# Optimization experiments

Measured on AMD Instinct MI355X. Metric: run time of the kernel, lower is better.

The kernel has to match this reference:

```python
import jax, jax.numpy as jnp
import numpy as np

WINDOW = 16  # hardcoded in module __init__

B, S, E, H = 2, 2048, 1024, 16
HD = E // H


def setup_inputs() -> dict:
    key = jax.random.key(0)
    k1, k2, k3, k4, k5, k6 = jax.random.split(key, 6)
    input_embeddings = jax.random.normal(k1, (B, S, E), dtype=jnp.float32)
    token_ids = jax.random.randint(k2, (B, S), 0, 32000, dtype=jnp.int64)
    # nn.MultiheadAttention parameters: packed in_proj (3E, E) + bias, out_proj (E, E) + bias
    in_proj_weight = jax.random.normal(k3, (3 * E, E), dtype=jnp.float32) * 0.02
    in_proj_bias = jax.random.normal(k4, (3 * E,), dtype=jnp.float32) * 0.02
    out_proj_weight = jax.random.normal(k5, (E, E), dtype=jnp.float32) * 0.02
    out_proj_bias = jax.random.normal(k6, (E,), dtype=jnp.float32) * 0.02
    return {
        "input_embeddings": input_embeddings,
        "token_ids": token_ids,
        "in_proj_weight": in_proj_weight,
        "in_proj_bias": in_proj_bias,
        "out_proj_weight": out_proj_weight,
        "out_proj_bias": out_proj_bias,
    }


def _blocked_mask(seq_len: int) -> jnp.ndarray:
    # Module sets mask[i, j] = True for j in [i - WINDOW, i] (17 positions).
    # PyTorch bool attn_mask: True = NOT allowed to attend.
    i = jnp.arange(seq_len)[:, None]
    j = jnp.arange(seq_len)[None, :]
    return (j <= i) & (j >= i - WINDOW)  # [S, S] bool, True = masked out


def reference(input_embeddings, token_ids, in_proj_weight, in_proj_bias,
              out_proj_weight, out_proj_bias):
    x = input_embeddings  # [B, S, E]
    b, s, e = x.shape
    # Packed QKV projection (torch Linear: y = x W^T + b)
    qkv = jnp.einsum('bse,fe->bsf', x, in_proj_weight) + in_proj_bias  # [B, S, 3E]
    q, k, v = jnp.split(qkv, 3, axis=-1)
    # Split heads: [B, H, S, HD]
    q = q.reshape(b, s, H, HD).transpose(0, 2, 1, 3)
    k = k.reshape(b, s, H, HD).transpose(0, 2, 1, 3)
    v = v.reshape(b, s, H, HD).transpose(0, 2, 1, 3)
    scale = 1.0 / jnp.sqrt(jnp.asarray(HD, dtype=x.dtype))
    scores = jnp.einsum('bhqd,bhkd->bhqk', q * scale, k)  # [B, H, S, S]
    blocked = _blocked_mask(s)  # True = masked
    scores = jnp.where(blocked[None, None, :, :], -jnp.inf, scores)
    attn = jax.nn.softmax(scores, axis=-1)
    ctx = jnp.einsum('bhqk,bhkd->bhqd', attn, v)  # [B, H, S, HD]
    ctx = ctx.transpose(0, 2, 1, 3).reshape(b, s, e)
    out = jnp.einsum('bse,fe->bsf', ctx, out_proj_weight) + out_proj_bias
    return out
```

## Files before the change

### kernel.cpp

```cpp
#include <hip/hip_runtime.h>

typedef __attribute__((ext_vector_type(8))) __bf16 bf16x8;
typedef __attribute__((ext_vector_type(4))) float f32x4;
typedef unsigned short u16;
typedef unsigned int u32;

#define MFMA16(a, b, c) __builtin_amdgcn_mfma_f32_16x16x32_bf16((a), (b), (c), 0, 0, 0)

__device__ __forceinline__ u16 f2bf(float f) {
  return (u16)((__float_as_uint(f) + 0x8000u) >> 16);
}

#define BDIM 2
#define SDIM 2048
#define EDIM 1024
#define HDIM 16
#define HD 64
#define MDIM (BDIM * SDIM)

#define SC_C1 0.1803368801111355f

typedef __attribute__((address_space(3))) void lds_void;
typedef __attribute__((address_space(1))) void g_void;

__device__ __forceinline__ void async_lds16(const void* g, void* lds_byte) {
  __builtin_amdgcn_global_load_lds((const g_void*)g, (lds_void*)lds_byte, 16, 0, 0);
}

__global__ __launch_bounds__(256) void cvt3_kernel(
    const float* __restrict__ s0, u16* __restrict__ d0, int n0,
    const float* __restrict__ s1, u16* __restrict__ d1, int n1,
    const float* __restrict__ s2, u16* __restrict__ d2, int n2) {
  int i = (blockIdx.x * 256 + threadIdx.x) * 8;
  const float* s;
  u16* d;
  if (i < n0) {
    s = s0 + i; d = d0 + i;
  } else if (i < n0 + n1) {
    s = s1 + (i - n0); d = d1 + (i - n0);
  } else if (i < n0 + n1 + n2) {
    s = s2 + (i - n0 - n1); d = d2 + (i - n0 - n1);
  } else {
    return;
  }
  float4 f0 = *(const float4*)(s);
  float4 f1 = *(const float4*)(s + 4);
  union { uint4 u; u16 h[8]; } o;
  o.h[0] = f2bf(f0.x); o.h[1] = f2bf(f0.y); o.h[2] = f2bf(f0.z); o.h[3] = f2bf(f0.w);
  o.h[4] = f2bf(f1.x); o.h[5] = f2bf(f1.y); o.h[6] = f2bf(f1.z); o.h[7] = f2bf(f1.w);
  *(uint4*)(d) = o.u;
}

__global__ __launch_bounds__(256) void gemm_qkv_kernel(
    const u16* __restrict__ X, const u16* __restrict__ W,
    const float* __restrict__ bias, u16* __restrict__ qb,
    u16* __restrict__ kb, u16* __restrict__ vtb) {
  __shared__ __align__(16) u16 As[128 * 64];
  __shared__ __align__(16) u16 Bs[128 * 64];
  const int m0 = blockIdx.x * 128, n0 = blockIdx.y * 128;
  const bool isV = (n0 >= 2 * EDIM);
  const int t = threadIdx.x;
  const int l = t & 63;
  const int quad = l >> 4, col = l & 15;
  const int wid = t >> 6;
  const int mh = wid & 1, nh = wid >> 1;
  const int wofs = (t & 192) << 4;
  f32x4 acc[4][4] = {};
  const u16* Ab = X + (size_t)m0 * EDIM;
  const u16* Bb = W + (size_t)n0 * EDIM;
  char* AsB = (char*)As;
  char* BsB = (char*)Bs;

  for (int k0 = 0; k0 < EDIM; k0 += 64) {
    __syncthreads();
#pragma unroll
    for (int p = 0; p < 4; p++) {
      int idx = p * 256 + t;
      int row = idx >> 3;
      int gch = (idx & 7) ^ (row & 7);
      async_lds16(Ab + (size_t)row * EDIM + k0 + gch * 8, AsB + p * 4096 + wofs);
      async_lds16(Bb + (size_t)row * EDIM + k0 + gch * 8, BsB + p * 4096 + wofs);
    }
    __syncthreads();
#pragma unroll
    for (int kk = 0; kk < 2; kk++) {
      bf16x8 af[4], bfr[4];
#pragma unroll
      for (int i = 0; i < 4; i++) {
        int ra = 64 * mh + 16 * i + col;
        af[i] = *(const bf16x8*)&As[ra * 64 + (((kk * 4 + quad) ^ (ra & 7)) * 8)];
        int rb = 64 * nh + 16 * i + col;
        bfr[i] = *(const bf16x8*)&Bs[rb * 64 + (((kk * 4 + quad) ^ (rb & 7)) * 8)];
      }
      if (isV) {
#pragma unroll
        for (int i = 0; i < 4; i++)
#pragma unroll
          for (int j = 0; j < 4; j++)
            acc[i][j] = MFMA16(bfr[i], af[j], acc[i][j]);
      } else {
#pragma unroll
        for (int i = 0; i < 4; i++)
#pragma unroll
          for (int j = 0; j < 4; j++)
            acc[i][j] = MFMA16(af[i], bfr[j], acc[i][j]);
      }
    }
  }

  if (isV) {
#pragma unroll
    for (int i = 0; i < 4; i++)
#pragma unroll
      for (int j = 0; j < 4; j++)
#pragma unroll
        for (int r = 0; r < 4; r++) {
          int n = n0 + 64 * nh + 16 * i + quad * 4 + r;
          int m = m0 + 64 * mh + 16 * j + col;
          float val = acc[i][j][r] + bias[n];
          int e = n & 1023;
          int hh = e >> 6, d = e & 63;
          int bb = m >> 11, s = m & 2047;
          vtb[(((size_t)(bb * HDIM + hh)) * HD + d) * SDIM + s] = f2bf(val);
        }
  } else {
    const float qscale = (n0 < EDIM) ? SC_C1 : 1.0f;
#pragma unroll
    for (int i = 0; i < 4; i++)
#pragma unroll
      for (int j = 0; j < 4; j++)
#pragma unroll
        for (int r = 0; r < 4; r++) {
          int m = m0 + 64 * mh + 16 * i + quad * 4 + r;
          int n = n0 + 64 * nh + 16 * j + col;
          float val = (acc[i][j][r] + bias[n]) * qscale;
          int which = n >> 10, e = n & 1023;
          int hh = e >> 6, d = e & 63;
          int bb = m >> 11, s = m & 2047;
          u16* dst = (which == 0) ? qb : kb;
          dst[(((size_t)(bb * HDIM + hh)) * SDIM + s) * HD + d] = f2bf(val);
        }
  }
}

__global__ __launch_bounds__(256) void attn_kernel(
    const u16* __restrict__ qg, const u16* __restrict__ kg,
    const u16* __restrict__ vtg, u16* __restrict__ ctx) {
  __shared__ __align__(16) u16 KB[2][64 * 64];
  __shared__ __align__(16) u16 VB[3][64 * 64];
  __shared__ __align__(16) u16 Ps[64 * 68];

  const int bh = blockIdx.x;
  const int q0 = blockIdx.y * 64;
  const int t = threadIdx.x;
  const int wid = t >> 6, l = t & 63;
  const int quad = l >> 4, col = l & 15;
  const size_t base = (size_t)bh * SDIM * HD;

  bf16x8 aq[2];
  {
    const u16* qp = qg + base + (size_t)(q0 + 16 * wid + col) * HD + quad * 8;
    aq[0] = *(const bf16x8*)(qp);
    aq[1] = *(const bf16x8*)(qp + 32);
  }
  const int qrow = q0 + 16 * wid + quad * 4;

  const int srow = t >> 3;
  const int g = (t & 7) ^ (srow & 7);
  const u16* kptr = kg + base + (size_t)srow * HD + g * 8;
  const u16* vptr = vtg + base + (size_t)srow * SDIM + g * 8;
  const int wofs = (t & 192) << 4;

  auto stageK = [&](int kt, int buf) {
    char* d = (char*)KB[buf] + wofs;
    async_lds16(kptr + (size_t)(kt * 64) * HD, d);
    async_lds16(kptr + (size_t)(kt * 64 + 32) * HD, d + 4096);
  };
  auto stageV = [&](int kt, int buf) {
    char* d = (char*)VB[buf] + wofs;
    async_lds16(vptr + kt * 64, d);
    async_lds16(vptr + (size_t)32 * SDIM + kt * 64, d + 4096);
  };
  auto qkt = [&](const u16* Kt, f32x4* sco) {
#pragma unroll
    for (int half = 0; half < 2; half++)
#pragma unroll
      for (int ct = 0; ct < 4; ct++) {
        int r = 16 * ct + col;
        int phys = (4 * half + quad) ^ (r & 7);
        bf16x8 bfrag = *(const bf16x8*)&Kt[r * 64 + phys * 8];
        sco[ct] = MFMA16(aq[half], bfrag, sco[ct]);
      }
  };

  float psum[4] = {};
  f32x4 oacc[4] = {};
  f32x4 sc[4] = {}, scn[4];

  const int NT = SDIM / 64;
  stageK(0, 0);
  stageV(0, 0);
  __syncthreads();
  qkt(KB[0], sc);
  stageK(1, 1);
  stageV(1, 1);

  int vb_n = 2;
  for (int kt = 0; kt < NT; kt++) {
    __syncthreads();
    if (kt + 1 < NT) {
#pragma unroll
      for (int ct = 0; ct < 4; ct++) scn[ct] = f32x4{0.f, 0.f, 0.f, 0.f};
      qkt(KB[(kt + 1) & 1], scn);
    }
    if (kt + 2 < NT) {
      stageK(kt + 2, kt & 1);
      stageV(kt + 2, vb_n);
    }
    vb_n = (vb_n == 2) ? 0 : vb_n + 1;

    const int k0 = kt * 64;
    const int pbase = (16 * wid + quad * 4) * 68 + col;
    if (k0 <= q0 + 63 && k0 + 63 >= q0 - 16) {
#pragma unroll
      for (int ct = 0; ct < 4; ct++)
#pragma unroll
        for (int r = 0; r < 4; r++) {
          int i = qrow + r, j = k0 + 16 * ct + col;
          float arg = (j <= i && j + 16 >= i) ? -1.0e30f : sc[ct][r];
          float p = __builtin_exp2f(arg);
          psum[r] += p;
          Ps[pbase + r * 68 + 16 * ct] = f2bf(p);
        }
    } else {
#pragma unroll
      for (int ct = 0; ct < 4; ct++)
#pragma unroll
        for (int r = 0; r < 4; r++) {
          float p = __builtin_exp2f(sc[ct][r]);
          psum[r] += p;
          Ps[pbase + r * 68 + 16 * ct] = f2bf(p);
        }
    }

    const u16* Vt = VB[kt % 3];
#pragma unroll
    for (int half = 0; half < 2; half++) {
      bf16x8 pa =
          *(const bf16x8*)&Ps[(16 * wid + col) * 68 + half * 32 + quad * 8];
#pragma unroll
      for (int dt = 0; dt < 4; dt++) {
        int vr = 16 * dt + col;
        int phys = (4 * half + quad) ^ (vr & 7);
        bf16x8 vbf = *(const bf16x8*)&Vt[vr * 64 + phys * 8];
        oacc[dt] = MFMA16(pa, vbf, oacc[dt]);
      }
    }
#pragma unroll
    for (int ct = 0; ct < 4; ct++) sc[ct] = scn[ct];
  }

#pragma unroll
  for (int off = 1; off < 16; off <<= 1)
#pragma unroll
    for (int r = 0; r < 4; r++) psum[r] += __shfl_xor(psum[r], off, 64);

  const int b = bh >> 4, h = bh & 15;
  float linv[4];
#pragma unroll
  for (int r = 0; r < 4; r++) linv[r] = 1.0f / psum[r];
#pragma unroll
  for (int dt = 0; dt < 4; dt++)
#pragma unroll
    for (int r = 0; r < 4; r++) {
      int qgl = qrow + r;
      int d = 16 * dt + col;
      ctx[((size_t)(b * SDIM + qgl)) * EDIM + h * HD + d] =
          f2bf(oacc[dt][r] * linv[r]);
    }
}

__global__ __launch_bounds__(256) void gemm_out_kernel(
    const u16* __restrict__ A, const u16* __restrict__ W,
    const float* __restrict__ bias, float* __restrict__ out) {
  __shared__ __align__(16) u16 As[128 * 64];
  __shared__ __align__(16) u16 Bs[128 * 64];
  const int m0 = blockIdx.x * 128, n0 = blockIdx.y * 128;
  const int t = threadIdx.x;
  const int l = t & 63;
  const int quad = l >> 4, col = l & 15;
  const int wid = t >> 6;
  const int mh = wid & 1, nh = wid >> 1;
  const int wofs = (t & 192) << 4;
  f32x4 acc[4][4] = {};
  const u16* Ab = A + (size_t)m0 * EDIM;
  const u16* Bb = W + (size_t)n0 * EDIM;
  char* AsB = (char*)As;
  char* BsB = (char*)Bs;

  for (int k0 = 0; k0 < EDIM; k0 += 64) {
    __syncthreads();
#pragma unroll
    for (int p = 0; p < 4; p++) {
      int idx = p * 256 + t;
      int row = idx >> 3;
      int gch = (idx & 7) ^ (row & 7);
      async_lds16(Ab + (size_t)row * EDIM + k0 + gch * 8, AsB + p * 4096 + wofs);
      async_lds16(Bb + (size_t)row * EDIM + k0 + gch * 8, BsB + p * 4096 + wofs);
    }
    __syncthreads();
#pragma unroll
    for (int kk = 0; kk < 2; kk++) {
      bf16x8 af[4], bfr[4];
#pragma unroll
      for (int i = 0; i < 4; i++) {
        int ra = 64 * mh + 16 * i + col;
        af[i] = *(const bf16x8*)&As[ra * 64 + (((kk * 4 + quad) ^ (ra & 7)) * 8)];
        int rb = 64 * nh + 16 * i + col;
        bfr[i] = *(const bf16x8*)&Bs[rb * 64 + (((kk * 4 + quad) ^ (rb & 7)) * 8)];
      }
#pragma unroll
      for (int i = 0; i < 4; i++)
#pragma unroll
        for (int j = 0; j < 4; j++)
          acc[i][j] = MFMA16(af[i], bfr[j], acc[i][j]);
    }
  }

#pragma unroll
  for (int i = 0; i < 4; i++)
#pragma unroll
    for (int j = 0; j < 4; j++)
#pragma unroll
      for (int r = 0; r < 4; r++) {
        int m = m0 + 64 * mh + 16 * i + quad * 4 + r;
        int n = n0 + 64 * nh + 16 * j + col;
        out[(size_t)m * EDIM + n] = acc[i][j][r] + bias[n];
      }
}

extern "C" void kernel_launch(void* const* d_in, const int* in_sizes, int n_in,
                              void* d_out, int out_size, void* d_ws,
                              size_t ws_size, hipStream_t stream) {
  const float* x = (const float*)d_in[0];
  const float* in_w = (const float*)d_in[2];
  const float* in_b = (const float*)d_in[3];
  const float* out_w = (const float*)d_in[4];
  const float* out_b = (const float*)d_in[5];
  float* out = (float*)d_out;

  char* ws = (char*)d_ws;
  u16* Xb  = (u16*)ws;
  u16* ctx = (u16*)ws;
  u16* qb  = (u16*)(ws + (size_t)( 8 << 20));
  u16* kb  = (u16*)(ws + (size_t)(16 << 20));
  u16* vtb = (u16*)(ws + (size_t)(24 << 20));
  u16* Wib = (u16*)(ws + (size_t)(32 << 20));
  u16* Wob = (u16*)(ws + (size_t)(38 << 20));

  const int nX = MDIM * EDIM;
  const int nWi = 3 * EDIM * EDIM;
  const int nWo = EDIM * EDIM;
  cvt3_kernel<<<(nX + nWi + nWo) / 8 / 256, 256, 0, stream>>>(
      x, Xb, nX, in_w, Wib, nWi, out_w, Wob, nWo);

  gemm_qkv_kernel<<<dim3(MDIM / 128, 3 * EDIM / 128), 256, 0, stream>>>(
      Xb, Wib, in_b, qb, kb, vtb);
  attn_kernel<<<dim3(BDIM * HDIM, SDIM / 64), 256, 0, stream>>>(qb, kb, vtb, ctx);
  gemm_out_kernel<<<dim3(MDIM / 128, EDIM / 128), 256, 0, stream>>>(
      ctx, Wob, out_b, out);
}
```

Measured before the change: 215.1 us.

## Transpose QK^T MFMA, swizzle P tile, double-buffer V, ping-pong score registers

The QK^T MFMA operands are swapped, so each lane holds scores for a single query row. The softmax row sum then becomes a per-lane scalar reduced with two shuffles, and P can be packed with v_cvt_pk_bf16_f32 into 8-byte swizzled LDS stores instead of scalar 2-byte stores. V staging goes from a triple buffer to a double buffer issued one tile ahead, and the loop is unrolled by two so the current/next score arrays alternate without register copies. The aim is to cut LDS store count, bank conflicts, VALU work and register moves, at the cost of less prefetch distance for V.

```diff
diff --git a/kernel.cpp b/kernel.cpp
--- a/kernel.cpp
+++ b/kernel.cpp
@@ -147,8 +147,8 @@
     const u16* __restrict__ qg, const u16* __restrict__ kg,
     const u16* __restrict__ vtg, u16* __restrict__ ctx) {
   __shared__ __align__(16) u16 KB[2][64 * 64];
-  __shared__ __align__(16) u16 VB[3][64 * 64];
-  __shared__ __align__(16) u16 Ps[64 * 68];
+  __shared__ __align__(16) u16 VB[2][64 * 64];
+  __shared__ __align__(16) u16 Ps[64 * 64];
 
   const int bh = blockIdx.x;
   const int q0 = blockIdx.y * 64;
@@ -163,6 +163,7 @@
     aq[0] = *(const bf16x8*)(qp);
     aq[1] = *(const bf16x8*)(qp + 32);
   }
+  const int qi = q0 + 16 * wid + col;
   const int qrow = q0 + 16 * wid + quad * 4;
 
   const int srow = t >> 3;
@@ -181,6 +182,7 @@
     async_lds16(vptr + kt * 64, d);
     async_lds16(vptr + (size_t)32 * SDIM + kt * 64, d + 4096);
   };
+
   auto qkt = [&](const u16* Kt, f32x4* sco) {
 #pragma unroll
     for (int half = 0; half < 2; half++)
@@ -188,87 +190,100 @@
       for (int ct = 0; ct < 4; ct++) {
         int r = 16 * ct + col;
         int phys = (4 * half + quad) ^ (r & 7);
-        bf16x8 bfrag = *(const bf16x8*)&Kt[r * 64 + phys * 8];
-        sco[ct] = MFMA16(aq[half], bfrag, sco[ct]);
-      }
-  };
-
-  float psum[4] = {};
+        bf16x8 kf = *(const bf16x8*)&Kt[r * 64 + phys * 8];
+        sco[ct] = MFMA16(kf, aq[half], sco[ct]);
+      }
+  };
+
+  char* PsB = (char*)Ps;
+  const int prow = 16 * wid + col;
+  int wPs[4], rPs[2];
+#pragma unroll
+  for (int ct = 0; ct < 4; ct++)
+    wPs[ct] = prow * 128 + (((2 * ct + (quad >> 1)) ^ (col & 7)) * 16) +
+              (quad & 1) * 8;
+#pragma unroll
+  for (int half = 0; half < 2; half++)
+    rPs[half] = prow * 128 + (((half * 4 + quad) ^ (col & 7)) * 16);
+
+  float psum = 0.f;
   f32x4 oacc[4] = {};
-  f32x4 sc[4] = {}, scn[4];
+  f32x4 scA[4] = {}, scB[4];
+
+  auto smax = [&](int kt, f32x4 (&cur)[4], bool band) {
+#pragma unroll
+    for (int ct = 0; ct < 4; ct++) {
+      float p[4];
+#pragma unroll
+      for (int r = 0; r < 4; r++) {
+        float s = cur[ct][r];
+        if (band) {
+          int j = kt * 64 + 16 * ct + quad * 4 + r;
+          if (j <= qi && j + 16 >= qi) s = -1.0e30f;
+        }
+        p[r] = __builtin_exp2f(s);
+        psum += p[r];
+      }
+      u32 w0, w1;
+      asm("v_cvt_pk_bf16_f32 %0, %1, %2" : "=v"(w0) : "v"(p[0]), "v"(p[1]));
+      asm("v_cvt_pk_bf16_f32 %0, %1, %2" : "=v"(w1) : "v"(p[2]), "v"(p[3]));
+      uint2 w;
+      w.x = w0;
+      w.y = w1;
+      *(uint2*)(PsB + wPs[ct]) = w;
+    }
+  };
+
+  auto pv = [&](const u16* Vt) {
+#pragma unroll
+    for (int half = 0; half < 2; half++) {
+      bf16x8 pa = *(const bf16x8*)(PsB + rPs[half]);
+#pragma unroll
+      for (int dt = 0; dt < 4; dt++) {
+        int vr = 16 * dt + col;
+        int phys = (4 * half + quad) ^ (vr & 7);
+        bf16x8 vf = *(const bf16x8*)&Vt[vr * 64 + phys * 8];
+        oacc[dt] = MFMA16(pa, vf, oacc[dt]);
+      }
+    }
+  };
 
   const int NT = SDIM / 64;
+
+  auto body = [&](int kt, f32x4 (&cur)[4], f32x4 (&nxt)[4]) {
+    __syncthreads();
+    if (kt + 2 < NT) stageK(kt + 2, kt & 1);
+    if (kt + 1 < NT) {
+      stageV(kt + 1, (kt + 1) & 1);
+#pragma unroll
+      for (int ct = 0; ct < 4; ct++) nxt[ct] = f32x4{0.f, 0.f, 0.f, 0.f};
+      qkt(KB[(kt + 1) & 1], nxt);
+    }
+    bool band = (kt * 64 <= q0 + 63) && (kt * 64 + 63 >= q0 - 16);
+    smax(kt, cur, band);
+    pv(VB[kt & 1]);
+  };
+
   stageK(0, 0);
   stageV(0, 0);
   __syncthreads();
-  qkt(KB[0], sc);
+  qkt(KB[0], scA);
   stageK(1, 1);
-  stageV(1, 1);
-
-  int vb_n = 2;
-  for (int kt = 0; kt < NT; kt++) {
-    __syncthreads();
-    if (kt + 1 < NT) {
-#pragma unroll
-      for (int ct = 0; ct < 4; ct++) scn[ct] = f32x4{0.f, 0.f, 0.f, 0.f};
-      qkt(KB[(kt + 1) & 1], scn);
-    }
-    if (kt + 2 < NT) {
-      stageK(kt + 2, kt & 1);
-      stageV(kt + 2, vb_n);
-    }
-    vb_n = (vb_n == 2) ? 0 : vb_n + 1;
-
-    const int k0 = kt * 64;
-    const int pbase = (16 * wid + quad * 4) * 68 + col;
-    if (k0 <= q0 + 63 && k0 + 63 >= q0 - 16) {
-#pragma unroll
-      for (int ct = 0; ct < 4; ct++)
-#pragma unroll
-        for (int r = 0; r < 4; r++) {
-          int i = qrow + r, j = k0 + 16 * ct + col;
-          float arg = (j <= i && j + 16 >= i) ? -1.0e30f : sc[ct][r];
-          float p = __builtin_exp2f(arg);
-          psum[r] += p;
-          Ps[pbase + r * 68 + 16 * ct] = f2bf(p);
-        }
-    } else {
-#pragma unroll
-      for (int ct = 0; ct < 4; ct++)
-#pragma unroll
-        for (int r = 0; r < 4; r++) {
-          float p = __builtin_exp2f(sc[ct][r]);
-          psum[r] += p;
-          Ps[pbase + r * 68 + 16 * ct] = f2bf(p);
-        }
-    }
-
-    const u16* Vt = VB[kt % 3];
-#pragma unroll
-    for (int half = 0; half < 2; half++) {
-      bf16x8 pa =
-          *(const bf16x8*)&Ps[(16 * wid + col) * 68 + half * 32 + quad * 8];
-#pragma unroll
-      for (int dt = 0; dt < 4; dt++) {
-        int vr = 16 * dt + col;
-        int phys = (4 * half + quad) ^ (vr & 7);
-        bf16x8 vbf = *(const bf16x8*)&Vt[vr * 64 + phys * 8];
-        oacc[dt] = MFMA16(pa, vbf, oacc[dt]);
-      }
-    }
-#pragma unroll
-    for (int ct = 0; ct < 4; ct++) sc[ct] = scn[ct];
-  }
-
-#pragma unroll
-  for (int off = 1; off < 16; off <<= 1)
-#pragma unroll
-    for (int r = 0; r < 4; r++) psum[r] += __shfl_xor(psum[r], off, 64);
+
+#pragma unroll 1
+  for (int kt = 0; kt < NT; kt += 2) {
+    body(kt, scA, scB);
+    body(kt + 1, scB, scA);
+  }
+
+  psum += __shfl_xor(psum, 16, 64);
+  psum += __shfl_xor(psum, 32, 64);
 
   const int b = bh >> 4, h = bh & 15;
   float linv[4];
 #pragma unroll
-  for (int r = 0; r < 4; r++) linv[r] = 1.0f / psum[r];
+  for (int r = 0; r < 4; r++)
+    linv[r] = 1.0f / __shfl(psum, quad * 4 + r, 64);
 #pragma unroll
   for (int dt = 0; dt < 4; dt++)
 #pragma unroll
```

New measurement: 221.0 us. 1.03x slower.
